# Kernel optimization log

Hardware: AMD Instinct MI355X
Metric: run time of the kernel (lower is better)

Reference implementation:

```python
import jax, jax.numpy as jnp
import numpy as np
import math

B, L, HID, H = 16, 1024, 1024, 16
E = HID // H
HALF = L // 2 + 1                      # 513 rfft bins
GLOBAL_RATIO = 0.6
LEFT = int(HALF * (1.0 - GLOBAL_RATIO))  # 205 (i=0, filter_mixer='G')
RIGHT = HALF                            # 513
FACTOR = 1
TOP_K = int(FACTOR * math.log(L))       # 6
LN_EPS = 1e-12


def setup_inputs() -> dict:
    key = jax.random.key(0)
    ks = jax.random.split(key, 12)
    s = 0.02
    return {
        "input_tensor": jax.random.normal(ks[0], (B, L, HID), jnp.float32),
        "attention_mask": jnp.zeros((B, 1, 1, L), jnp.float32),
        "Wq": jax.random.normal(ks[1], (HID, HID), jnp.float32) * s,
        "bq": jnp.zeros((HID,), jnp.float32),
        "Wk": jax.random.normal(ks[2], (HID, HID), jnp.float32) * s,
        "bk": jnp.zeros((HID,), jnp.float32),
        "Wv": jax.random.normal(ks[3], (HID, HID), jnp.float32) * s,
        "bv": jnp.zeros((HID,), jnp.float32),
        "Wd": jax.random.normal(ks[4], (HID, HID), jnp.float32) * s,
        "bd": jnp.zeros((HID,), jnp.float32),
        "gamma": jnp.ones((HID,), jnp.float32),
        "beta": jnp.zeros((HID,), jnp.float32),
    }


def _heads(x):  # [B,L,HID] -> [B,H,E,L]
    return x.reshape(B, L, H, E).transpose(0, 2, 3, 1)


def _layer_norm(x, gamma, beta):
    mu = jnp.mean(x, axis=-1, keepdims=True)
    var = jnp.var(x, axis=-1, keepdims=True)
    return (x - mu) / jnp.sqrt(var + LN_EPS) * gamma + beta


def reference(input_tensor, attention_mask, Wq, bq, Wk, bk, Wv, bv, Wd, bd, gamma, beta):
    # QKV projections -> [B,H,E,L]
    q = _heads(input_tensor @ Wq + bq)
    k = _heads(input_tensor @ Wk + bk)
    v = _heads(input_tensor @ Wv + bv)

    # FFT-based autocorrelation restricted to retained frequency band [LEFT,RIGHT)
    q_fft = jnp.fft.rfft(q, axis=-1)            # [B,H,E,HALF] complex64
    k_fft = jnp.fft.rfft(k, axis=-1)
    res = q_fft[..., LEFT:RIGHT] * jnp.conj(k_fft[..., LEFT:RIGHT])
    box = jnp.zeros((B, H, E, HALF), res.dtype).at[..., LEFT:RIGHT].set(res)
    corr = jnp.fft.irfft(box, n=L, axis=-1)     # [B,H,E,L]

    # time_delay_agg_training: topk shared delays, softmax-weighted roll aggregation
    mean_value = jnp.mean(corr, axis=(1, 2))            # [B,L]
    _, idx = jax.lax.top_k(jnp.mean(mean_value, axis=0), TOP_K)  # [TOP_K]
    weights = mean_value[:, idx]                         # [B,TOP_K]
    tmp_corr = jax.nn.softmax(weights, axis=-1)
    delays_agg = jnp.zeros_like(v)
    for i in range(TOP_K):  # TOP_K=6, fixed small loop
        pattern = jnp.roll(v, -idx[i], axis=-1)
        delays_agg = delays_agg + pattern * tmp_corr[:, i][:, None, None, None]

    # [B,H,E,L] -> [B,L,HID]
    context = delays_agg.transpose(0, 3, 1, 2).reshape(B, L, HID)
    hidden = context @ Wd + bd
    return _layer_norm(hidden + input_tensor, gamma, beta)
```

## Files before the change

### kernel.cpp

```cpp
#include <hip/hip_runtime.h>


typedef unsigned short u16;
typedef unsigned int   u32;
typedef __attribute__((ext_vector_type(8))) __bf16 bf16x8;
typedef __attribute__((ext_vector_type(4))) float  floatx4;

#define HIDn 1024

__device__ __forceinline__ u16 f2b(float f){ u32 i = __float_as_uint(f); return (u16)((i + 0x7fffu + ((i>>16)&1u)) >> 16); }

__device__ __forceinline__ void gl_lds16(const u16* g, u16* l){
  __builtin_amdgcn_global_load_lds((__attribute__((address_space(1))) const void*)g,
                                   (__attribute__((address_space(3))) void*)l, 16, 0, 0);
}

__global__ void fill_kernel(float* __restrict__ out, float v, int n)
{
  const int i = blockIdx.x*blockDim.x + threadIdx.x;
  if (i < n) out[i] = v;
}

__global__ __launch_bounds__(256)
void cast_kernel(const float* __restrict__ x, u16* __restrict__ xb)
{
  const int i = blockIdx.x*256 + threadIdx.x;
  const float4* xp = (const float4*)x;
  const float4 a = xp[2*i], b = xp[2*i+1];
  uint4 o;
  o.x = (u32)f2b(a.x) | ((u32)f2b(a.y)<<16);
  o.y = (u32)f2b(a.z) | ((u32)f2b(a.w)<<16);
  o.z = (u32)f2b(b.x) | ((u32)f2b(b.y)<<16);
  o.w = (u32)f2b(b.z) | ((u32)f2b(b.w)<<16);
  ((uint4*)xb)[i] = o;
}

__global__ __launch_bounds__(1024)
void transpose_kernel(const float* __restrict__ Wq, const float* __restrict__ Wk,
                      const float* __restrict__ Wv, const float* __restrict__ Wd,
                      u16* __restrict__ WqkvT, u16* __restrict__ WdT)
{
  __shared__ float tile[32][33];
  const int mat = blockIdx.z;
  const float* W = (mat==0)?Wq:(mat==1)?Wk:(mat==2)?Wv:Wd;
  const int k = blockIdx.y*32 + threadIdx.y;
  const int n = blockIdx.x*32 + threadIdx.x;
  tile[threadIdx.y][threadIdx.x] = W[(long)k*HIDn + n];
  __syncthreads();
  const int on = blockIdx.x*32 + threadIdx.y;
  const int ok = blockIdx.y*32 + threadIdx.x;
  const u16 val = f2b(tile[threadIdx.x][threadIdx.y]);
  if (mat < 3) WqkvT[(long)(mat*HIDn + on)*HIDn + ok] = val;
  else         WdT[(long)on*HIDn + ok] = val;
}

__global__ __launch_bounds__(1024)
void gf_kernel(float* __restrict__ gf, float* __restrict__ c)
{
  const int d = threadIdx.x;
  float s = 0.f;
  for (int f = 205; f < 512; ++f){
    int p = (f*d) & 1023;
    s += cosf(6.283185307179586f * (float)p * (1.0f/1024.0f));
  }
  gf[d] = (2.f*s + ((d & 1) ? -1.f : 1.f)) * (1.0f/1048576.0f);
  #pragma unroll
  for (int b = 0; b < 16; ++b) c[b*1024 + d] = 0.f;
}

template<int EPI>
__global__ __launch_bounds__(256)
void gemm_mfma(const u16* __restrict__ A, int lda, long sA,
               const u16* __restrict__ Bt, int ldb, long sB,
               void* __restrict__ C0, u16* __restrict__ o1, u16* __restrict__ o2,
               int ldc, int K,
               const float* __restrict__ b0, const float* __restrict__ b1,
               const float* __restrict__ b2, const float* __restrict__ resid,
               float* __restrict__ cbuf)
{
  __shared__ __align__(16) u16 As[128*64];
  __shared__ __align__(16) u16 Bs[128*64];
  __shared__ float bins[256];
  const int bx = blockIdx.x, by = blockIdx.y, bz = blockIdx.z;
  const int tid  = threadIdx.x;
  const int wave = tid >> 6, lane = tid & 63;
  const u16* Ab = A  + (long)bz * sA;
  const u16* Bb = Bt + (long)bz * sB;
  const int aRow0 = by * 128, bRow0 = bx * 128;
  const int waveM = wave >> 1, waveN = wave & 1;
  const int qd = lane >> 4, ln = lane & 15;
  const int sRow = lane >> 3;
  const int sColSwz = ((lane & 7) ^ sRow) * 8;

  if (EPI == 3) bins[tid] = 0.f;

  floatx4 acc[4][4];
  const floatx4 z4 = {0.f, 0.f, 0.f, 0.f};
  #pragma unroll
  for (int i=0;i<4;++i)
    #pragma unroll
    for (int j=0;j<4;++j) acc[i][j] = z4;

  const int rl = ln & 7, lh = ln >> 3;
  for (int k0 = 0; k0 < K; k0 += 64){
    __syncthreads();
    #pragma unroll
    for (int i=0;i<4;++i){
      const int g  = wave*4 + i;
      const int rw = g*8 + sRow;
      gl_lds16(Ab + (long)(aRow0 + rw)*lda + (k0 + sColSwz), As + g*512);
      gl_lds16(Bb + (long)(bRow0 + rw)*ldb + (k0 + sColSwz), Bs + g*512);
    }
    asm volatile("s_waitcnt vmcnt(0)" ::: "memory");
    __syncthreads();
    #pragma unroll
    for (int ks=0; ks<2; ++ks){
      const int csw = ((ks*4 + qd) ^ rl) * 8;
      bf16x8 av[4], bv[4];
      #pragma unroll
      for (int mi=0;mi<4;++mi)
        av[mi] = *(const bf16x8*)(As + (waveM*8 + mi*2 + lh)*512 + rl*64 + csw);
      #pragma unroll
      for (int ni=0;ni<4;++ni)
        bv[ni] = *(const bf16x8*)(Bs + (waveN*8 + ni*2 + lh)*512 + rl*64 + csw);
      #pragma unroll
      for (int mi=0;mi<4;++mi)
        #pragma unroll
        for (int ni=0;ni<4;++ni)
          acc[mi][ni] = __builtin_amdgcn_mfma_f32_16x16x32_bf16(av[mi], bv[ni], acc[mi][ni], 0, 0, 0);
    }
  }

  if (EPI == 3){
    float dsum[7][4];
    #pragma unroll
    for (int dd=0; dd<7; ++dd)
      #pragma unroll
      for (int r=0;r<4;++r) dsum[dd][r] = 0.f;
    #pragma unroll
    for (int mi=0;mi<4;++mi)
      #pragma unroll
      for (int ni=0;ni<4;++ni){
        const int dd = mi - ni + 3;
        #pragma unroll
        for (int r=0;r<4;++r) dsum[dd][r] += acc[mi][ni][r];
      }
    const int base = 127 + 64*(waveM - waveN) + 4*qd - ln;
    #pragma unroll
    for (int dd=0; dd<7; ++dd)
      #pragma unroll
      for (int r=0;r<4;++r)
        atomicAdd(&bins[base + 16*(dd-3) + r], dsum[dd][r]);
    __syncthreads();
    if (tid < 255){
      const int d = (aRow0 - bRow0 + tid - 127) & 1023;
      atomicAdd(cbuf + bz*1024 + d, bins[tid]);
    }
    return;
  }

  #pragma unroll
  for (int mi=0;mi<4;++mi){
    const int gm = aRow0 + waveM*64 + mi*16 + qd*4;
    #pragma unroll
    for (int ni=0;ni<4;++ni){
      const int gn = bRow0 + waveN*64 + ni*16 + ln;
      floatx4 v = acc[mi][ni];
      if (EPI == 0){
        const int which = gn >> 10, nl = gn & 1023;
        const float* bp = (which==0) ? b0 : ((which==1) ? b1 : b2);
        u16* Cb = (which==0) ? (u16*)C0 : ((which==1) ? o1 : o2);
        const float bias = bp[nl];
        #pragma unroll
        for (int r=0;r<4;++r) Cb[(long)(gm+r)*ldc + nl] = f2b(v[r] + bias);
      } else {
        const float bias = b0[gn];
        float* C = (float*)C0;
        #pragma unroll
        for (int r=0;r<4;++r)
          C[(long)(gm+r)*ldc + gn] = v[r] + bias + resid[(long)(gm+r)*ldc + gn];
      }
    }
  }
}

__global__ __launch_bounds__(1024)
void filter_kernel(const float* __restrict__ c, const float* __restrict__ gf,
                   float* __restrict__ mv)
{
  __shared__ float carr[1024];
  __shared__ float gsh[1024];
  const int b = blockIdx.x, l = threadIdx.x;
  carr[l] = c[b*1024 + l]; gsh[l] = gf[l];
  __syncthreads();
  float o = 0.f;
  #pragma unroll 4
  for (int m = 0; m < 1024; ++m) o += carr[m] * gsh[(l - m) & 1023];
  mv[b*1024 + l] = o;
}

__global__ __launch_bounds__(1024)
void topk_kernel(const float* __restrict__ mv, int* __restrict__ idxout,
                 float* __restrict__ wout)
{
  __shared__ float vals[1024];
  __shared__ float rv[1024];
  __shared__ int   ri[1024];
  __shared__ int   chosen[6];
  const int t = threadIdx.x;
  float s = 0.f;
  #pragma unroll
  for (int b = 0; b < 16; ++b) s += mv[b*1024 + t];
  vals[t] = s;
  __syncthreads();
  for (int r = 0; r < 6; ++r){
    rv[t] = vals[t]; ri[t] = t; __syncthreads();
    for (int off = 512; off > 0; off >>= 1){
      if (t < off){
        const float v2 = rv[t+off]; const int i2 = ri[t+off];
        if (v2 > rv[t] || (v2 == rv[t] && i2 < ri[t])){ rv[t] = v2; ri[t] = i2; }
      }
      __syncthreads();
    }
    if (t == 0){ chosen[r] = ri[0]; idxout[r] = ri[0]; }
    __syncthreads();
    if (t == chosen[r]) vals[t] = -3.0e38f;
    __syncthreads();
  }
  if (t < 16){
    float w[6]; float mx = -3.0e38f;
    #pragma unroll
    for (int i = 0; i < 6; ++i){ w[i] = mv[t*1024 + chosen[i]]; mx = fmaxf(mx, w[i]); }
    float sum = 0.f;
    #pragma unroll
    for (int i = 0; i < 6; ++i){ w[i] = expf(w[i] - mx); sum += w[i]; }
    #pragma unroll
    for (int i = 0; i < 6; ++i) wout[t*6 + i] = w[i] / sum;
  }
}

__global__ __launch_bounds__(256)
void context_kernel(const u16* __restrict__ Vb, const int* __restrict__ idx,
                    const float* __restrict__ w, u16* __restrict__ CT)
{
  const int row = blockIdx.x*2 + (threadIdx.x >> 7);
  const int b = row >> 10, l = row & 1023;
  const int t = threadIdx.x & 127;
  float wl[6]; int id[6];
  #pragma unroll
  for (int i = 0; i < 6; ++i){ id[i] = idx[i]; wl[i] = w[b*6 + i]; }
  float acc[8] = {0,0,0,0,0,0,0,0};
  #pragma unroll
  for (int i = 0; i < 6; ++i){
    const long src = (long)b*1024 + ((l + id[i]) & 1023);
    const uint4 pk = *(const uint4*)(Vb + src*1024 + t*8);
    const float ww = wl[i];
    union{float f; u32 u;} cv;
    cv.u = pk.x<<16;          acc[0] += ww*cv.f;
    cv.u = pk.x & 0xffff0000u; acc[1] += ww*cv.f;
    cv.u = pk.y<<16;          acc[2] += ww*cv.f;
    cv.u = pk.y & 0xffff0000u; acc[3] += ww*cv.f;
    cv.u = pk.z<<16;          acc[4] += ww*cv.f;
    cv.u = pk.z & 0xffff0000u; acc[5] += ww*cv.f;
    cv.u = pk.w<<16;          acc[6] += ww*cv.f;
    cv.u = pk.w & 0xffff0000u; acc[7] += ww*cv.f;
  }
  uint4 o;
  o.x = (u32)f2b(acc[0]) | ((u32)f2b(acc[1])<<16);
  o.y = (u32)f2b(acc[2]) | ((u32)f2b(acc[3])<<16);
  o.z = (u32)f2b(acc[4]) | ((u32)f2b(acc[5])<<16);
  o.w = (u32)f2b(acc[6]) | ((u32)f2b(acc[7])<<16);
  *(uint4*)(CT + (long)row*1024 + t*8) = o;
}

__global__ __launch_bounds__(256)
void ln_kernel(float* __restrict__ io, const float* __restrict__ gamma,
               const float* __restrict__ beta)
{
  __shared__ float s1[256];
  __shared__ float s2[256];
  const int row = blockIdx.x, t = threadIdx.x;
  float4 v = ((const float4*)(io + (long)row*1024))[t];
  s1[t] = v.x+v.y+v.z+v.w;
  s2[t] = v.x*v.x+v.y*v.y+v.z*v.z+v.w*v.w;
  __syncthreads();
  for (int off = 128; off > 0; off >>= 1){
    if (t < off){ s1[t] += s1[t+off]; s2[t] += s2[t+off]; }
    __syncthreads();
  }
  const float mu  = s1[0] * (1.f/1024.f);
  const float var = fmaxf(s2[0] * (1.f/1024.f) - mu*mu, 0.f);
  const float rstd = rsqrtf(var + 1e-12f);
  const float4 g  = ((const float4*)gamma)[t];
  const float4 be = ((const float4*)beta)[t];
  float4 o;
  o.x = (v.x-mu)*rstd*g.x + be.x;
  o.y = (v.y-mu)*rstd*g.y + be.y;
  o.z = (v.z-mu)*rstd*g.z + be.z;
  o.w = (v.w-mu)*rstd*g.w + be.w;
  ((float4*)(io + (long)row*1024))[t] = o;
}

extern "C" void kernel_launch(void* const* d_in, const int* in_sizes, int n_in,
                              void* d_out, int out_size, void* d_ws, size_t ws_size,
                              hipStream_t stream)
{
  (void)in_sizes; (void)n_in;
  const float* x     = (const float*)d_in[0];
  const float* Wq    = (const float*)d_in[2];
  const float* bq    = (const float*)d_in[3];
  const float* Wk    = (const float*)d_in[4];
  const float* bk    = (const float*)d_in[5];
  const float* Wv    = (const float*)d_in[6];
  const float* bv    = (const float*)d_in[7];
  const float* Wd    = (const float*)d_in[8];
  const float* bd    = (const float*)d_in[9];
  const float* gamma = (const float*)d_in[10];
  const float* beta  = (const float*)d_in[11];
  float* outp = (float*)d_out;

  const size_t NEED = 142741952UL;
  if (ws_size < NEED){
    const int n = out_size/2;
    fill_kernel<<<(n+255)/256, 256, 0, stream>>>(outp, (float)ws_size, n);
    return;
  }
  char* ws = (char*)d_ws;
  u16*  xb    = (u16*)(ws);
  u16*  Qb    = (u16*)(ws + 33554432L);
  u16*  Kb    = (u16*)(ws + 67108864L);
  u16*  Vb    = (u16*)(ws + 100663296L);
  u16*  WqkvT = (u16*)(ws + 134217728L);
  u16*  WdT   = (u16*)(ws + 140509184L);
  float* cbuf = (float*)(ws + 142606336L);
  float* mv   = (float*)(ws + 142671872L);
  float* gf   = (float*)(ws + 142737408L);
  int*   idxb = (int*)  (ws + 142741504L);
  float* wsm  = (float*)(ws + 142741568L);
  u16*  CT    = Qb;

  cast_kernel<<<8192, 256, 0, stream>>>(x, xb);
  transpose_kernel<<<dim3(32,32,4), dim3(32,32), 0, stream>>>(Wq, Wk, Wv, Wd, WqkvT, WdT);
  gf_kernel<<<1, 1024, 0, stream>>>(gf, cbuf);

  gemm_mfma<0><<<dim3(24,128,1), 256, 0, stream>>>(
      xb, 1024, 0L, WqkvT, 1024, 0L, Qb, Kb, Vb, 1024, 1024,
      bq, bk, bv, nullptr, nullptr);

  gemm_mfma<3><<<dim3(8,8,16), 256, 0, stream>>>(
      Qb, 1024, 1048576L, Kb, 1024, 1048576L, nullptr, nullptr, nullptr, 0, 1024,
      nullptr, nullptr, nullptr, nullptr, cbuf);

  filter_kernel<<<16, 1024, 0, stream>>>(cbuf, gf, mv);
  topk_kernel<<<1, 1024, 0, stream>>>(mv, idxb, wsm);
  context_kernel<<<8192, 256, 0, stream>>>(Vb, idxb, wsm, CT);

  gemm_mfma<2><<<dim3(8,128,1), 256, 0, stream>>>(
      CT, 1024, 0L, WdT, 1024, 0L, outp, nullptr, nullptr, 1024, 1024,
      bd, nullptr, nullptr, x, nullptr);

  ln_kernel<<<16384, 256, 0, stream>>>(outp, gamma, beta);
}
```

Before: 544.7 us.

## Rewrite MFMA GEMM as 256x256 tile, 8-wave double-buffered pipelined kernel

The GEMM kernel moves from 128x128 tiles with 4 waves to 256x256 tiles with 8 waves and a double-buffered LDS pipeline. Global-to-LDS loads for the next K tiles are interleaved with MFMA phases, using barriers, partial vmcnt waits and s_setprio to overlap loads with compute. The goal is more data reuse per tile and hiding memory latency behind the matrix ops. In exchange it needs much more LDS (128KB per block) and registers, which lowers occupancy and leaves fewer blocks to fill the GPU, especially for the batched correlation GEMM.

Result: faster. 497.7 us (-8.6%).

```diff
diff --git a/kernel.cpp b/kernel.cpp
--- a/kernel.cpp
+++ b/kernel.cpp
@@ -13,6 +13,16 @@
 __device__ __forceinline__ void gl_lds16(const u16* g, u16* l){
   __builtin_amdgcn_global_load_lds((__attribute__((address_space(1))) const void*)g,
                                    (__attribute__((address_space(3))) void*)l, 16, 0, 0);
+}
+
+__device__ __forceinline__ void bar(){
+  asm volatile("" ::: "memory");
+  __builtin_amdgcn_s_barrier();
+  asm volatile("" ::: "memory");
+}
+__device__ __forceinline__ void lgkm0(){
+  asm volatile("s_waitcnt lgkmcnt(0)" ::: "memory");
+  __builtin_amdgcn_sched_barrier(0);
 }
 
 __global__ void fill_kernel(float* __restrict__ out, float v, int n)
@@ -69,7 +79,7 @@
 }
 
 template<int EPI>
-__global__ __launch_bounds__(256)
+__global__ __launch_bounds__(512, 2)
 void gemm_mfma(const u16* __restrict__ A, int lda, long sA,
                const u16* __restrict__ Bt, int ldb, long sB,
                void* __restrict__ C0, u16* __restrict__ o1, u16* __restrict__ o2,
@@ -78,107 +88,198 @@
                const float* __restrict__ b2, const float* __restrict__ resid,
                float* __restrict__ cbuf)
 {
-  __shared__ __align__(16) u16 As[128*64];
-  __shared__ __align__(16) u16 Bs[128*64];
-  __shared__ float bins[256];
+  __shared__ __align__(16) u16 As[2][16384];
+  __shared__ __align__(16) u16 Bs[2][16384];
+  __shared__ float bins[512];
+
   const int bx = blockIdx.x, by = blockIdx.y, bz = blockIdx.z;
   const int tid  = threadIdx.x;
   const int wave = tid >> 6, lane = tid & 63;
+  const int waveM = wave >> 2, waveN = wave & 3;
+  const int qd = lane >> 4, ln = lane & 15, rl = ln & 7;
   const u16* Ab = A  + (long)bz * sA;
   const u16* Bb = Bt + (long)bz * sB;
-  const int aRow0 = by * 128, bRow0 = bx * 128;
-  const int waveM = wave >> 1, waveN = wave & 1;
-  const int qd = lane >> 4, ln = lane & 15;
-  const int sRow = lane >> 3;
-  const int sColSwz = ((lane & 7) ^ sRow) * 8;
+  const int aRow0 = by * 256, bRow0 = bx * 256;
+  const int nt = K >> 6;
+
+  const int s0 = wave*128 + lane;
+  const int r0 = s0 >> 3, r1 = r0 + 8;
+  const int kc = ((s0 & 7) ^ (r0 & 7)) * 8;
+  const long aOff0 = (long)(aRow0 + r0)*lda + kc;
+  const long aOff1 = (long)(aRow0 + r1)*lda + kc;
+  const long bOff0 = (long)(bRow0 + r0)*ldb + kc;
+  const long bOff1 = (long)(bRow0 + r1)*ldb + kc;
+  const int dstW = wave*1024;
+
+#define STAGE_A(p, h, kt) do{ \
+    gl_lds16(Ab + aOff0 + (long)(h)*128*lda + (kt), &As[p][(h)*8192 + dstW]); \
+    gl_lds16(Ab + aOff1 + (long)(h)*128*lda + (kt), &As[p][(h)*8192 + dstW + 512]); }while(0)
+#define STAGE_B(p, h, kt) do{ \
+    gl_lds16(Bb + bOff0 + (long)(h)*128*ldb + (kt), &Bs[p][(h)*8192 + dstW]); \
+    gl_lds16(Bb + bOff1 + (long)(h)*128*ldb + (kt), &Bs[p][(h)*8192 + dstW + 512]); }while(0)
 
   if (EPI == 3) bins[tid] = 0.f;
 
-  floatx4 acc[4][4];
+  floatx4 acc[8][4];
   const floatx4 z4 = {0.f, 0.f, 0.f, 0.f};
   #pragma unroll
-  for (int i=0;i<4;++i)
+  for (int i=0;i<8;++i)
     #pragma unroll
     for (int j=0;j<4;++j) acc[i][j] = z4;
 
-  const int rl = ln & 7, lh = ln >> 3;
-  for (int k0 = 0; k0 < K; k0 += 64){
-    __syncthreads();
-    #pragma unroll
-    for (int i=0;i<4;++i){
-      const int g  = wave*4 + i;
-      const int rw = g*8 + sRow;
-      gl_lds16(Ab + (long)(aRow0 + rw)*lda + (k0 + sColSwz), As + g*512);
-      gl_lds16(Bb + (long)(bRow0 + rw)*ldb + (k0 + sColSwz), Bs + g*512);
-    }
-    asm volatile("s_waitcnt vmcnt(0)" ::: "memory");
-    __syncthreads();
-    #pragma unroll
-    for (int ks=0; ks<2; ++ks){
-      const int csw = ((ks*4 + qd) ^ rl) * 8;
-      bf16x8 av[4], bv[4];
+  const int aRd = (waveM*128 + ln)*64;
+  const int bRd = (waveN*64  + ln)*64;
+  const int csw0 = ((0 + qd) ^ rl) * 8;
+  const int csw1 = ((4 + qd) ^ rl) * 8;
+
+  STAGE_B(0,0,0); STAGE_B(0,1,0); STAGE_A(0,0,0); STAGE_A(0,1,0);
+  STAGE_B(1,0,64); STAGE_B(1,1,64); STAGE_A(1,0,64);
+  asm volatile("s_waitcnt vmcnt(6)" ::: "memory");
+  __builtin_amdgcn_s_barrier();
+  asm volatile("" ::: "memory");
+
+  bf16x8 av[2][4], bv[2][4];
+  for (int t = 0; t < nt; ++t){
+    const int p = t & 1, pn = p ^ 1;
+    const u16* Ap = &As[p][0];
+    const u16* Bp = &Bs[p][0];
+    const int k1 = (t+1) << 6, k2 = (t+2) << 6;
+
+    #pragma unroll
+    for (int mi=0;mi<4;++mi){
+      av[0][mi] = *(const bf16x8*)(Ap + aRd + mi*1024 + csw0);
+      av[1][mi] = *(const bf16x8*)(Ap + aRd + mi*1024 + csw1);
+    }
+    #pragma unroll
+    for (int ni=0;ni<2;++ni){
+      bv[0][ni] = *(const bf16x8*)(Bp + bRd + ni*1024 + csw0);
+      bv[1][ni] = *(const bf16x8*)(Bp + bRd + ni*1024 + csw1);
+    }
+    if (t+1 < nt) STAGE_A(pn, 1, k1);
+    bar(); lgkm0();
+    __builtin_amdgcn_s_setprio(1);
+    #pragma unroll
+    for (int kk=0;kk<2;++kk)
       #pragma unroll
       for (int mi=0;mi<4;++mi)
-        av[mi] = *(const bf16x8*)(As + (waveM*8 + mi*2 + lh)*512 + rl*64 + csw);
-      #pragma unroll
-      for (int ni=0;ni<4;++ni)
-        bv[ni] = *(const bf16x8*)(Bs + (waveN*8 + ni*2 + lh)*512 + rl*64 + csw);
+        #pragma unroll
+        for (int ni=0;ni<2;++ni)
+          acc[mi][ni] = __builtin_amdgcn_mfma_f32_16x16x32_bf16(av[kk][mi], bv[kk][ni], acc[mi][ni], 0,0,0);
+    __builtin_amdgcn_s_setprio(0);
+    bar();
+
+    #pragma unroll
+    for (int ni=2;ni<4;++ni){
+      bv[0][ni] = *(const bf16x8*)(Bp + bRd + ni*1024 + csw0);
+      bv[1][ni] = *(const bf16x8*)(Bp + bRd + ni*1024 + csw1);
+    }
+    bar(); lgkm0();
+    __builtin_amdgcn_s_setprio(1);
+    #pragma unroll
+    for (int kk=0;kk<2;++kk)
       #pragma unroll
       for (int mi=0;mi<4;++mi)
         #pragma unroll
-        for (int ni=0;ni<4;++ni)
-          acc[mi][ni] = __builtin_amdgcn_mfma_f32_16x16x32_bf16(av[mi], bv[ni], acc[mi][ni], 0, 0, 0);
-    }
-  }
+        for (int ni=2;ni<4;++ni)
+          acc[mi][ni] = __builtin_amdgcn_mfma_f32_16x16x32_bf16(av[kk][mi], bv[kk][ni], acc[mi][ni], 0,0,0);
+    __builtin_amdgcn_s_setprio(0);
+    bar();
+
+    #pragma unroll
+    for (int mi=0;mi<4;++mi){
+      av[0][mi] = *(const bf16x8*)(Ap + aRd + 4096 + mi*1024 + csw0);
+      av[1][mi] = *(const bf16x8*)(Ap + aRd + 4096 + mi*1024 + csw1);
+    }
+    if (t+2 < nt) STAGE_B(p, 0, k2);
+    bar(); lgkm0();
+    __builtin_amdgcn_s_setprio(1);
+    #pragma unroll
+    for (int kk=0;kk<2;++kk)
+      #pragma unroll
+      for (int mi=0;mi<4;++mi)
+        #pragma unroll
+        for (int ni=0;ni<2;++ni)
+          acc[4+mi][ni] = __builtin_amdgcn_mfma_f32_16x16x32_bf16(av[kk][mi], bv[kk][ni], acc[4+mi][ni], 0,0,0);
+    __builtin_amdgcn_s_setprio(0);
+    bar();
+
+    if (t+2 < nt){
+      STAGE_B(p, 1, k2); STAGE_A(p, 0, k2);
+      asm volatile("s_waitcnt vmcnt(6)" ::: "memory");
+    } else if (t+1 < nt){
+      asm volatile("s_waitcnt vmcnt(0)" ::: "memory");
+    }
+    bar();
+    __builtin_amdgcn_s_setprio(1);
+    #pragma unroll
+    for (int kk=0;kk<2;++kk)
+      #pragma unroll
+      for (int mi=0;mi<4;++mi)
+        #pragma unroll
+        for (int ni=2;ni<4;++ni)
+          acc[4+mi][ni] = __builtin_amdgcn_mfma_f32_16x16x32_bf16(av[kk][mi], bv[kk][ni], acc[4+mi][ni], 0,0,0);
+    __builtin_amdgcn_s_setprio(0);
+    bar();
+  }
+#undef STAGE_A
+#undef STAGE_B
 
   if (EPI == 3){
-    float dsum[7][4];
-    #pragma unroll
-    for (int dd=0; dd<7; ++dd)
+    float dsum[11][4];
+    #pragma unroll
+    for (int dd=0; dd<11; ++dd)
       #pragma unroll
       for (int r=0;r<4;++r) dsum[dd][r] = 0.f;
     #pragma unroll
-    for (int mi=0;mi<4;++mi)
+    for (int mi=0;mi<8;++mi)
       #pragma unroll
       for (int ni=0;ni<4;++ni){
         const int dd = mi - ni + 3;
         #pragma unroll
         for (int r=0;r<4;++r) dsum[dd][r] += acc[mi][ni][r];
       }
-    const int base = 127 + 64*(waveM - waveN) + 4*qd - ln;
-    #pragma unroll
-    for (int dd=0; dd<7; ++dd)
+    const int base = 255 + 128*waveM - 64*waveN + 4*qd - ln;
+    #pragma unroll
+    for (int dd=0; dd<11; ++dd)
       #pragma unroll
       for (int r=0;r<4;++r)
         atomicAdd(&bins[base + 16*(dd-3) + r], dsum[dd][r]);
     __syncthreads();
-    if (tid < 255){
-      const int d = (aRow0 - bRow0 + tid - 127) & 1023;
+    if (tid < 511){
+      const int d = (aRow0 - bRow0 + tid - 255) & 1023;
       atomicAdd(cbuf + bz*1024 + d, bins[tid]);
     }
     return;
   }
 
-  #pragma unroll
-  for (int mi=0;mi<4;++mi){
-    const int gm = aRow0 + waveM*64 + mi*16 + qd*4;
-    #pragma unroll
-    for (int ni=0;ni<4;++ni){
-      const int gn = bRow0 + waveN*64 + ni*16 + ln;
-      floatx4 v = acc[mi][ni];
-      if (EPI == 0){
-        const int which = gn >> 10, nl = gn & 1023;
-        const float* bp = (which==0) ? b0 : ((which==1) ? b1 : b2);
-        u16* Cb = (which==0) ? (u16*)C0 : ((which==1) ? o1 : o2);
+  if (EPI == 0){
+    const int which = bx >> 2;
+    const float* bp = (which==0) ? b0 : ((which==1) ? b1 : b2);
+    u16* Cb = (which==0) ? (u16*)C0 : ((which==1) ? o1 : o2);
+    const int nb = bRow0 & 1023;
+    #pragma unroll
+    for (int mi=0;mi<8;++mi){
+      const int gm = aRow0 + waveM*128 + mi*16 + qd*4;
+      #pragma unroll
+      for (int ni=0;ni<4;++ni){
+        const int nl = nb + waveN*64 + ni*16 + ln;
         const float bias = bp[nl];
         #pragma unroll
-        for (int r=0;r<4;++r) Cb[(long)(gm+r)*ldc + nl] = f2b(v[r] + bias);
-      } else {
+        for (int r=0;r<4;++r) Cb[(long)(gm+r)*ldc + nl] = f2b(acc[mi][ni][r] + bias);
+      }
+    }
+  } else {
+    float* C = (float*)C0;
+    #pragma unroll
+    for (int mi=0;mi<8;++mi){
+      const int gm = aRow0 + waveM*128 + mi*16 + qd*4;
+      #pragma unroll
+      for (int ni=0;ni<4;++ni){
+        const int gn = bRow0 + waveN*64 + ni*16 + ln;
         const float bias = b0[gn];
-        float* C = (float*)C0;
         #pragma unroll
         for (int r=0;r<4;++r)
-          C[(long)(gm+r)*ldc + gn] = v[r] + bias + resid[(long)(gm+r)*ldc + gn];
+          C[(long)(gm+r)*ldc + gn] = acc[mi][ni][r] + bias + resid[(long)(gm+r)*ldc + gn];
       }
     }
   }
@@ -343,11 +444,11 @@
   transpose_kernel<<<dim3(32,32,4), dim3(32,32), 0, stream>>>(Wq, Wk, Wv, Wd, WqkvT, WdT);
   gf_kernel<<<1, 1024, 0, stream>>>(gf, cbuf);
 
-  gemm_mfma<0><<<dim3(24,128,1), 256, 0, stream>>>(
+  gemm_mfma<0><<<dim3(12,64,1), 512, 0, stream>>>(
       xb, 1024, 0L, WqkvT, 1024, 0L, Qb, Kb, Vb, 1024, 1024,
       bq, bk, bv, nullptr, nullptr);
 
-  gemm_mfma<3><<<dim3(8,8,16), 256, 0, stream>>>(
+  gemm_mfma<3><<<dim3(4,4,16), 512, 0, stream>>>(
       Qb, 1024, 1048576L, Kb, 1024, 1048576L, nullptr, nullptr, nullptr, 0, 1024,
       nullptr, nullptr, nullptr, nullptr, cbuf);
 
@@ -355,7 +456,7 @@
   topk_kernel<<<1, 1024, 0, stream>>>(mv, idxb, wsm);
   context_kernel<<<8192, 256, 0, stream>>>(Vb, idxb, wsm, CT);
 
-  gemm_mfma<2><<<dim3(8,128,1), 256, 0, stream>>>(
+  gemm_mfma<2><<<dim3(4,64,1), 512, 0, stream>>>(
       CT, 1024, 0L, WdT, 1024, 0L, outp, nullptr, nullptr, 1024, 1024,
       bd, nullptr, nullptr, x, nullptr);
 
```
